# Kernel tuning notes

Hardware: AMD Instinct MI355X
Metric: run time of the kernel (lower is better)

Reference implementation:

```python
import jax, jax.numpy as jnp
import numpy as np

OUTPUT_BIT = 8
N_SCALE = 28          # scale_bits
EXP_BITS = 16
SEGMENTS = 16
DEGREE = 2
S_VAL = 0.03          # input quantization scale


def _fit_pieces(s):
    # Mirrors _compute_integer_coefficients for backend='float':
    # fit exp((x_off-127)*s) over offset domain x_off*s in [-128s, 127s].
    xs_off = np.linspace(-128.0, 127.0, 10000)
    ys = np.exp((xs_off - 127.0) * s)
    xs = xs_off * s
    bounds = np.linspace(-128.0 * s, 127.0 * s, SEGMENTS + 1)
    coeffs = np.zeros((SEGMENTS, DEGREE + 1))  # ascending powers a0,a1,a2
    for j in range(SEGMENTS):
        m = (xs >= bounds[j]) & (xs <= bounds[j + 1])
        coeffs[j] = np.polyfit(xs[m], ys[m], DEGREE)[::-1]
    # integer coefficients: p(x_int*s)*2^N = sum_k floor(a_k*s^k*2^N)*x_int^k
    pw = s ** np.arange(DEGREE + 1)
    coeffs_int = np.floor(coeffs * pw[None, :] * (2.0 ** N_SCALE))
    lo_int = np.floor(bounds[:-1] / s)  # integer segment lower bounds
    return lo_int.astype(np.float32), coeffs_int.astype(np.float32)


def setup_inputs() -> dict:
    key = jax.random.key(0)
    x = jax.random.normal(key, (8, 12, 512, 512), dtype=jnp.float32) * 4.0
    scaling_factor = jnp.full((1,), S_VAL, dtype=jnp.float32)
    lo_np, cf_np = _fit_pieces(S_VAL)
    return {
        "x": x,
        "scaling_factor": scaling_factor,
        "lo_bounds": jnp.asarray(lo_np),
        "coeffs": jnp.asarray(cf_np),
    }


def floor_ste(y):
    # floor with straight-through gradient
    return y + jax.lax.stop_gradient(jnp.floor(y) - y)


def reference(x, scaling_factor, lo_bounds, coeffs):
    s = scaling_factor
    x_int = floor_ste(x / s)
    x_int = x_int - jnp.max(x_int, axis=-1, keepdims=True) + 127.0

    # piecewise-polynomial integer exp (computed under no_grad in the original)
    xi = jax.lax.stop_gradient(x_int)
    idx = jnp.clip(jnp.searchsorted(lo_bounds, xi, side="right") - 1, 0, SEGMENTS - 1)
    c = coeffs[idx]                         # [..., deg+1], ascending powers
    r = c[..., DEGREE]
    for k in range(DEGREE - 1, -1, -1):     # Horner evaluation
        r = r * xi + c[..., k]
    exp_int = jnp.maximum(jax.lax.stop_gradient(r), 0.0)

    exp_int = floor_ste(exp_int / 2.0 ** (30 - EXP_BITS + 1))
    exp_sum = jnp.maximum(jnp.sum(exp_int, axis=-1, keepdims=True), 1.0)
    factor = jnp.floor(2.0 ** 32 / jax.lax.stop_gradient(exp_sum))
    softmax_int = jnp.floor(jax.lax.stop_gradient(exp_int) * factor / 2.0 ** (32 - OUTPUT_BIT + 1))

    softmax_float = jax.nn.softmax(x, axis=-1)
    s_out = jnp.array([2.0 / 2 ** OUTPUT_BIT], dtype=x.dtype)
    smi_f = softmax_int * s_out
    # STE: integer value forward, float-softmax gradient backward
    output = jax.lax.stop_gradient(smi_f) + (softmax_float - jax.lax.stop_gradient(softmax_float))
    output = s_out * floor_ste(output / s_out)
    return output, s_out
```

## Files before the change

### kernel.cpp

```cpp
#include <hip/hip_runtime.h>


#define ROWLEN 512

typedef float nfloat4 __attribute__((ext_vector_type(4)));

#define DPP_SUM_I32(t)                                                        \
    t += __builtin_amdgcn_update_dpp(0, t, 0x111, 0xf, 0xf, true);            \
    t += __builtin_amdgcn_update_dpp(0, t, 0x112, 0xf, 0xf, true);            \
    t += __builtin_amdgcn_update_dpp(0, t, 0x114, 0xf, 0xf, true);            \
    t += __builtin_amdgcn_update_dpp(0, t, 0x118, 0xf, 0xf, true);            \
    t += __builtin_amdgcn_update_dpp(0, t, 0x142, 0xa, 0xf, true);            \
    t += __builtin_amdgcn_update_dpp(0, t, 0x143, 0xc, 0xf, true);

#define DPP_MAX_F32_STEP(m, ctrl, rmask)                                      \
    {                                                                         \
        int _mi = __float_as_int(m);                                          \
        int _sh = __builtin_amdgcn_update_dpp(_mi, _mi, ctrl, rmask, 0xf, false); \
        m = fmaxf(m, __int_as_float(_sh));                                    \
    }
#define DPP_MIN_F32_STEP(m, ctrl, rmask)                                      \
    {                                                                         \
        int _mi = __float_as_int(m);                                          \
        int _sh = __builtin_amdgcn_update_dpp(_mi, _mi, ctrl, rmask, 0xf, false); \
        m = fminf(m, __int_as_float(_sh));                                    \
    }

__global__ __launch_bounds__(256) void lut_builder(
    const float* __restrict__ cf, int* __restrict__ glut)
{
    const int tid = threadIdx.x;
    int4 ev;
    int* evp = reinterpret_cast<int*>(&ev);
    const int j0 = tid * 4;
    #pragma unroll
    for (int jj = 0; jj < 4; ++jj) {
        const int j  = j0 + jj;
        const int u  = j - 768;
        const int uc = u < 0 ? 0 : u;
        int idx = ((uc + 1) * 257) >> 12;
        idx = idx > 15 ? 15 : idx;
        const int c0 = (int)cf[idx * 3 + 0];
        const int c1 = (int)cf[idx * 3 + 1];
        const int c2 = (int)cf[idx * 3 + 2];
        const int xi = j - 896;
        const int r1 = c2 * xi + c1;
        long long r2 = (long long)r1 * xi + c0;
        if (r2 < 0) r2 = 0;
        evp[jj] = (int)(r2 >> 15);
    }
    reinterpret_cast<int4*>(glut)[tid] = ev;
}

__global__ __launch_bounds__(256, 8) void ppis_kernel(
    const float* __restrict__ x,
    const float* __restrict__ sfp,
    const float* __restrict__ lo,
    const float* __restrict__ cf,
    float* __restrict__ out,
    const int* __restrict__ glut,
    int has_glut,
    int nrows)
{
    __shared__ int  s_e[1024];
    __shared__ int4 s_cf[16];

    const int tid  = threadIdx.x;
    const int lane = tid & 63;
    const int wid  = tid >> 6;

    const long long row = (long long)blockIdx.x * 4 + wid;
    const float4* xp = reinterpret_cast<const float4*>(x) + row * (ROWLEN / 4);
    const float4 va = xp[lane];
    const float4 vb = xp[lane + 64];

    const float s  = sfp[0];
    const float ry = 1.0f / s;

    if (tid < 16)
        s_cf[tid] = make_int4((int)cf[tid*3+0], (int)cf[tid*3+1], (int)cf[tid*3+2], 0);

    if (has_glut) {
        reinterpret_cast<int4*>(s_e)[tid] =
            reinterpret_cast<const int4*>(glut)[tid];
    } else {
        int4 ev;
        int* evp = reinterpret_cast<int*>(&ev);
        const int j0 = tid * 4;
        #pragma unroll
        for (int jj = 0; jj < 4; ++jj) {
            const int j  = j0 + jj;
            const int u  = j - 768;
            const int uc = u < 0 ? 0 : u;
            int idx = ((uc + 1) * 257) >> 12;
            idx = idx > 15 ? 15 : idx;
            const int c0 = (int)cf[idx * 3 + 0];
            const int c1 = (int)cf[idx * 3 + 1];
            const int c2 = (int)cf[idx * 3 + 2];
            const int xi = j - 896;
            const int r1 = c2 * xi + c1;
            long long r2 = (long long)r1 * xi + c0;
            if (r2 < 0) r2 = 0;
            evp[jj] = (int)(r2 >> 15);
        }
        reinterpret_cast<int4*>(s_e)[tid] = ev;
    }
    __syncthreads();

    const float xv[8] = {va.x, va.y, va.z, va.w, vb.x, vb.y, vb.z, vb.w};

    float mf = fmaxf(fmaxf(fmaxf(xv[0], xv[1]), fmaxf(xv[2], xv[3])),
                     fmaxf(fmaxf(xv[4], xv[5]), fmaxf(xv[6], xv[7])));
    float nf_ = fminf(fminf(fminf(xv[0], xv[1]), fminf(xv[2], xv[3])),
                      fminf(fminf(xv[4], xv[5]), fminf(xv[6], xv[7])));
    DPP_MAX_F32_STEP(mf, 0x111, 0xf)  DPP_MIN_F32_STEP(nf_, 0x111, 0xf)
    DPP_MAX_F32_STEP(mf, 0x112, 0xf)  DPP_MIN_F32_STEP(nf_, 0x112, 0xf)
    DPP_MAX_F32_STEP(mf, 0x114, 0xf)  DPP_MIN_F32_STEP(nf_, 0x114, 0xf)
    DPP_MAX_F32_STEP(mf, 0x118, 0xf)  DPP_MIN_F32_STEP(nf_, 0x118, 0xf)
    DPP_MAX_F32_STEP(mf, 0x142, 0xa)  DPP_MIN_F32_STEP(nf_, 0x142, 0xa)
    DPP_MAX_F32_STEP(mf, 0x143, 0xc)  DPP_MIN_F32_STEP(nf_, 0x143, 0xc)
    const float xmax = __int_as_float(__builtin_amdgcn_readlane(__float_as_int(mf), 63));
    const float xmin = __int_as_float(__builtin_amdgcn_readlane(__float_as_int(nf_), 63));

    auto fdiv_floor = [&](float xk) -> int {
        float nf = floorf(xk * ry);
        const float d = fmaf(-s, nf, xk);
        nf = (d < 0.0f) ? nf - 1.0f : nf;
        const float u = fmaf(-s, nf + 1.0f, xk);
        nf = (u >= 0.0f) ? nf + 1.0f : nf;
        return (int)nf;
    };

    int n[8];
    #pragma unroll
    for (int k = 0; k < 8; ++k) n[k] = fdiv_floor(xv[k]);
    const int mx = fdiv_floor(xmax);
    const int mn = fdiv_floor(xmin);

    const int joff = 1023 - mx;

    int e[8];
    int tsum = 0;
    if (mn + joff >= 0) {
        #pragma unroll
        for (int k = 0; k < 8; ++k) {
            e[k] = s_e[n[k] + joff];
            tsum += e[k];
        }
    } else {
        #pragma unroll
        for (int k = 0; k < 8; ++k) {
            const int u  = n[k] + (255 - mx);
            const int uc = u < 0 ? 0 : u;
            int idx = ((uc + 1) * 257) >> 12;
            idx = idx > 15 ? 15 : idx;
            const int4 c = s_cf[idx];
            const long long xi = (long long)(u - 128);
            long long r2 = ((long long)c.z * xi + c.y) * xi + c.x;
            if (r2 < 0) r2 = 0;
            e[k] = (int)(r2 >> 15);
            tsum += e[k];
        }
    }

    DPP_SUM_I32(tsum)
    int ts = __builtin_amdgcn_readlane(tsum, 63);
    if (ts < 1) ts = 1;

    const unsigned int factor =
        (unsigned int)floor(__ddiv_rn(4294967296.0, (double)ts));

    nfloat4 o0, o1;
    #pragma unroll
    for (int k = 0; k < 4; ++k) {
        const unsigned long long p0 = (unsigned long long)(unsigned int)e[k]   * factor;
        const unsigned long long p1 = (unsigned long long)(unsigned int)e[k+4] * factor;
        o0[k] = (float)(int)(p0 >> 25) * 0.0078125f;
        o1[k] = (float)(int)(p1 >> 25) * 0.0078125f;
    }

    nfloat4* op = reinterpret_cast<nfloat4*>(out) + row * (ROWLEN / 4);
    op[lane]      = o0;
    op[lane + 64] = o1;

    if (row == 0 && lane == 0)
        out[(long long)nrows * ROWLEN] = 0.0078125f;
}

extern "C" void kernel_launch(void* const* d_in, const int* in_sizes, int n_in,
                              void* d_out, int out_size, void* d_ws, size_t ws_size,
                              hipStream_t stream) {
    const float* x  = (const float*)d_in[0];
    const float* sf = (const float*)d_in[1];
    const float* lo = (const float*)d_in[2];
    const float* cf = (const float*)d_in[3];
    float* out = (float*)d_out;

    const int nrows = in_sizes[0] / ROWLEN;

    const int has_glut = (d_ws != nullptr && ws_size >= 4096) ? 1 : 0;
    int* glut = (int*)d_ws;
    if (has_glut)
        lut_builder<<<1, 256, 0, stream>>>(cf, glut);

    ppis_kernel<<<nrows / 4, 256, 0, stream>>>(x, sf, lo, cf, out,
                                               glut, has_glut, nrows);
}
```

Baseline: 184.3 us.

## Process four rows per single-wave block with software-prefetched row loads

Shrinks the block from four waves to one wave that handles four consecutive rows in sequence. Each block now loads the whole LUT into LDS itself and drops the __syncthreads. Loads for later rows are issued before earlier rows are processed, using sched_barrier to keep them early and overlap memory latency with compute. In exchange, each wave fills the full LUT and holds more registers for the prefetched rows, and the LDS fill relies on intra-wave ordering instead of a barrier.

```diff
diff --git a/kernel.cpp b/kernel.cpp
--- a/kernel.cpp
+++ b/kernel.cpp
@@ -52,7 +52,7 @@
     reinterpret_cast<int4*>(glut)[tid] = ev;
 }
 
-__global__ __launch_bounds__(256, 8) void ppis_kernel(
+__global__ __launch_bounds__(64, 8) void ppis_kernel(
     const float* __restrict__ x,
     const float* __restrict__ sfp,
     const float* __restrict__ lo,
@@ -65,14 +65,15 @@
     __shared__ int  s_e[1024];
     __shared__ int4 s_cf[16];
 
-    const int tid  = threadIdx.x;
-    const int lane = tid & 63;
-    const int wid  = tid >> 6;
-
-    const long long row = (long long)blockIdx.x * 4 + wid;
-    const float4* xp = reinterpret_cast<const float4*>(x) + row * (ROWLEN / 4);
-    const float4 va = xp[lane];
-    const float4 vb = xp[lane + 64];
+    const int tid = threadIdx.x;
+
+    const long long row0 = (long long)blockIdx.x * 4;
+    const float4* xp = reinterpret_cast<const float4*>(x) + row0 * (ROWLEN / 4);
+
+    float4 a0 = xp[tid];
+    float4 b0 = xp[tid + 64];
+    float4 a1 = xp[128 + tid];
+    float4 b1 = xp[128 + 64 + tid];
 
     const float s  = sfp[0];
     const float ry = 1.0f / s;
@@ -80,47 +81,39 @@
     if (tid < 16)
         s_cf[tid] = make_int4((int)cf[tid*3+0], (int)cf[tid*3+1], (int)cf[tid*3+2], 0);
 
+    int4* se4 = reinterpret_cast<int4*>(s_e);
     if (has_glut) {
-        reinterpret_cast<int4*>(s_e)[tid] =
-            reinterpret_cast<const int4*>(glut)[tid];
+        const int4* g4 = reinterpret_cast<const int4*>(glut);
+        int4 L0 = g4[tid], L1 = g4[tid + 64], L2 = g4[tid + 128], L3 = g4[tid + 192];
+        se4[tid]       = L0;
+        se4[tid + 64]  = L1;
+        se4[tid + 128] = L2;
+        se4[tid + 192] = L3;
     } else {
-        int4 ev;
-        int* evp = reinterpret_cast<int*>(&ev);
-        const int j0 = tid * 4;
         #pragma unroll
-        for (int jj = 0; jj < 4; ++jj) {
-            const int j  = j0 + jj;
-            const int u  = j - 768;
-            const int uc = u < 0 ? 0 : u;
-            int idx = ((uc + 1) * 257) >> 12;
-            idx = idx > 15 ? 15 : idx;
-            const int c0 = (int)cf[idx * 3 + 0];
-            const int c1 = (int)cf[idx * 3 + 1];
-            const int c2 = (int)cf[idx * 3 + 2];
-            const int xi = j - 896;
-            const int r1 = c2 * xi + c1;
-            long long r2 = (long long)r1 * xi + c0;
-            if (r2 < 0) r2 = 0;
-            evp[jj] = (int)(r2 >> 15);
+        for (int q = 0; q < 4; ++q) {
+            int4 ev;
+            int* evp = reinterpret_cast<int*>(&ev);
+            const int j0 = (tid + q * 64) * 4;
+            #pragma unroll
+            for (int jj = 0; jj < 4; ++jj) {
+                const int j  = j0 + jj;
+                const int u  = j - 768;
+                const int uc = u < 0 ? 0 : u;
+                int idx = ((uc + 1) * 257) >> 12;
+                idx = idx > 15 ? 15 : idx;
+                const int c0 = (int)cf[idx * 3 + 0];
+                const int c1 = (int)cf[idx * 3 + 1];
+                const int c2 = (int)cf[idx * 3 + 2];
+                const int xi = j - 896;
+                const int r1 = c2 * xi + c1;
+                long long r2 = (long long)r1 * xi + c0;
+                if (r2 < 0) r2 = 0;
+                evp[jj] = (int)(r2 >> 15);
+            }
+            se4[tid + q * 64] = ev;
         }
-        reinterpret_cast<int4*>(s_e)[tid] = ev;
-    }
-    __syncthreads();
-
-    const float xv[8] = {va.x, va.y, va.z, va.w, vb.x, vb.y, vb.z, vb.w};
-
-    float mf = fmaxf(fmaxf(fmaxf(xv[0], xv[1]), fmaxf(xv[2], xv[3])),
-                     fmaxf(fmaxf(xv[4], xv[5]), fmaxf(xv[6], xv[7])));
-    float nf_ = fminf(fminf(fminf(xv[0], xv[1]), fminf(xv[2], xv[3])),
-                      fminf(fminf(xv[4], xv[5]), fminf(xv[6], xv[7])));
-    DPP_MAX_F32_STEP(mf, 0x111, 0xf)  DPP_MIN_F32_STEP(nf_, 0x111, 0xf)
-    DPP_MAX_F32_STEP(mf, 0x112, 0xf)  DPP_MIN_F32_STEP(nf_, 0x112, 0xf)
-    DPP_MAX_F32_STEP(mf, 0x114, 0xf)  DPP_MIN_F32_STEP(nf_, 0x114, 0xf)
-    DPP_MAX_F32_STEP(mf, 0x118, 0xf)  DPP_MIN_F32_STEP(nf_, 0x118, 0xf)
-    DPP_MAX_F32_STEP(mf, 0x142, 0xa)  DPP_MIN_F32_STEP(nf_, 0x142, 0xa)
-    DPP_MAX_F32_STEP(mf, 0x143, 0xc)  DPP_MIN_F32_STEP(nf_, 0x143, 0xc)
-    const float xmax = __int_as_float(__builtin_amdgcn_readlane(__float_as_int(mf), 63));
-    const float xmin = __int_as_float(__builtin_amdgcn_readlane(__float_as_int(nf_), 63));
+    }
 
     auto fdiv_floor = [&](float xk) -> int {
         float nf = floorf(xk * ry);
@@ -131,59 +124,90 @@
         return (int)nf;
     };
 
-    int n[8];
-    #pragma unroll
-    for (int k = 0; k < 8; ++k) n[k] = fdiv_floor(xv[k]);
-    const int mx = fdiv_floor(xmax);
-    const int mn = fdiv_floor(xmin);
-
-    const int joff = 1023 - mx;
-
-    int e[8];
-    int tsum = 0;
-    if (mn + joff >= 0) {
+    nfloat4* ob = reinterpret_cast<nfloat4*>(out) + row0 * (ROWLEN / 4);
+
+    auto process = [&](const float4& va, const float4& vb, int obase) {
+        const float xv[8] = {va.x, va.y, va.z, va.w, vb.x, vb.y, vb.z, vb.w};
+
+        float mf = fmaxf(fmaxf(fmaxf(xv[0], xv[1]), fmaxf(xv[2], xv[3])),
+                         fmaxf(fmaxf(xv[4], xv[5]), fmaxf(xv[6], xv[7])));
+        float nf_ = fminf(fminf(fminf(xv[0], xv[1]), fminf(xv[2], xv[3])),
+                          fminf(fminf(xv[4], xv[5]), fminf(xv[6], xv[7])));
+        DPP_MAX_F32_STEP(mf, 0x111, 0xf)  DPP_MIN_F32_STEP(nf_, 0x111, 0xf)
+        DPP_MAX_F32_STEP(mf, 0x112, 0xf)  DPP_MIN_F32_STEP(nf_, 0x112, 0xf)
+        DPP_MAX_F32_STEP(mf, 0x114, 0xf)  DPP_MIN_F32_STEP(nf_, 0x114, 0xf)
+        DPP_MAX_F32_STEP(mf, 0x118, 0xf)  DPP_MIN_F32_STEP(nf_, 0x118, 0xf)
+        DPP_MAX_F32_STEP(mf, 0x142, 0xa)  DPP_MIN_F32_STEP(nf_, 0x142, 0xa)
+        DPP_MAX_F32_STEP(mf, 0x143, 0xc)  DPP_MIN_F32_STEP(nf_, 0x143, 0xc)
+        const float xmax = __int_as_float(__builtin_amdgcn_readlane(__float_as_int(mf), 63));
+        const float xmin = __int_as_float(__builtin_amdgcn_readlane(__float_as_int(nf_), 63));
+
+        int n[8];
         #pragma unroll
-        for (int k = 0; k < 8; ++k) {
-            e[k] = s_e[n[k] + joff];
-            tsum += e[k];
+        for (int k = 0; k < 8; ++k) n[k] = fdiv_floor(xv[k]);
+        const int mx = fdiv_floor(xmax);
+        const int mn = fdiv_floor(xmin);
+
+        const int joff = 1023 - mx;
+
+        int e[8];
+        int tsum = 0;
+        if (mn + joff >= 0) {
+            #pragma unroll
+            for (int k = 0; k < 8; ++k) {
+                e[k] = s_e[n[k] + joff];
+                tsum += e[k];
+            }
+        } else {
+            #pragma unroll
+            for (int k = 0; k < 8; ++k) {
+                const int u  = n[k] + (255 - mx);
+                const int uc = u < 0 ? 0 : u;
+                int idx = ((uc + 1) * 257) >> 12;
+                idx = idx > 15 ? 15 : idx;
+                const int4 c = s_cf[idx];
+                const long long xi = (long long)(u - 128);
+                long long r2 = ((long long)c.z * xi + c.y) * xi + c.x;
+                if (r2 < 0) r2 = 0;
+                e[k] = (int)(r2 >> 15);
+                tsum += e[k];
+            }
         }
-    } else {
+
+        DPP_SUM_I32(tsum)
+        int ts = __builtin_amdgcn_readlane(tsum, 63);
+        if (ts < 1) ts = 1;
+
+        const unsigned int factor =
+            (unsigned int)floor(__ddiv_rn(4294967296.0, (double)ts));
+
+        nfloat4 o0, o1;
         #pragma unroll
-        for (int k = 0; k < 8; ++k) {
-            const int u  = n[k] + (255 - mx);
-            const int uc = u < 0 ? 0 : u;
-            int idx = ((uc + 1) * 257) >> 12;
-            idx = idx > 15 ? 15 : idx;
-            const int4 c = s_cf[idx];
-            const long long xi = (long long)(u - 128);
-            long long r2 = ((long long)c.z * xi + c.y) * xi + c.x;
-            if (r2 < 0) r2 = 0;
-            e[k] = (int)(r2 >> 15);
-            tsum += e[k];
+        for (int k = 0; k < 4; ++k) {
+            const unsigned long long p0 = (unsigned long long)(unsigned int)e[k]   * factor;
+            const unsigned long long p1 = (unsigned long long)(unsigned int)e[k+4] * factor;
+            o0[k] = (float)(int)(p0 >> 25) * 0.0078125f;
+            o1[k] = (float)(int)(p1 >> 25) * 0.0078125f;
         }
-    }
-
-    DPP_SUM_I32(tsum)
-    int ts = __builtin_amdgcn_readlane(tsum, 63);
-    if (ts < 1) ts = 1;
-
-    const unsigned int factor =
-        (unsigned int)floor(__ddiv_rn(4294967296.0, (double)ts));
-
-    nfloat4 o0, o1;
-    #pragma unroll
-    for (int k = 0; k < 4; ++k) {
-        const unsigned long long p0 = (unsigned long long)(unsigned int)e[k]   * factor;
-        const unsigned long long p1 = (unsigned long long)(unsigned int)e[k+4] * factor;
-        o0[k] = (float)(int)(p0 >> 25) * 0.0078125f;
-        o1[k] = (float)(int)(p1 >> 25) * 0.0078125f;
-    }
-
-    nfloat4* op = reinterpret_cast<nfloat4*>(out) + row * (ROWLEN / 4);
-    op[lane]      = o0;
-    op[lane + 64] = o1;
-
-    if (row == 0 && lane == 0)
+
+        ob[obase + tid]      = o0;
+        ob[obase + tid + 64] = o1;
+    };
+
+    float4 a2 = xp[256 + tid];
+    float4 b2 = xp[256 + 64 + tid];
+    __builtin_amdgcn_sched_barrier(0);
+    process(a0, b0, 0);
+
+    float4 a3 = xp[384 + tid];
+    float4 b3 = xp[384 + 64 + tid];
+    __builtin_amdgcn_sched_barrier(0);
+    process(a1, b1, 128);
+
+    process(a2, b2, 256);
+    process(a3, b3, 384);
+
+    if (row0 == 0 && tid == 0)
         out[(long long)nrows * ROWLEN] = 0.0078125f;
 }
 
@@ -203,6 +227,6 @@
     if (has_glut)
         lut_builder<<<1, 256, 0, stream>>>(cf, glut);
 
-    ppis_kernel<<<nrows / 4, 256, 0, stream>>>(x, sf, lo, cf, out,
-                                               glut, has_glut, nrows);
+    ppis_kernel<<<nrows / 4, 64, 0, stream>>>(x, sf, lo, cf, out,
+                                              glut, has_glut, nrows);
 }
```

After: 190.4 us. 3.3% more time.
